# Kernel tuning notes

Hardware: AMD Instinct MI355X
Metric: run time of the kernel (lower is better)

Reference implementation:

```python
import jax, jax.numpy as jnp
import numpy as np

T = 2048
N = 4096
DT = 0.01
V_RESET = 1.0
ALPHA = 0.01
MAX_SPIKES = 128


def setup_inputs() -> dict:
    key = jax.random.key(0)
    ks = jax.random.split(key, 8)
    ts = jnp.arange(T, dtype=jnp.float32) * DT
    input_current = jax.random.normal(ks[0], (T, N), dtype=jnp.float32)
    # _build_w: uniform(minval=0.5) fully-connected weight matrix
    w = jax.random.uniform(ks[1], (N, N), dtype=jnp.float32, minval=0.5, maxval=1.0)
    # _build_initial: uniform(maxval=0.1)
    v0 = jax.random.uniform(ks[2], (N,), dtype=jnp.float32, maxval=0.1)
    i0 = jax.random.uniform(ks[3], (N,), dtype=jnp.float32, maxval=0.1)
    mu = jax.random.uniform(ks[4], (2,), dtype=jnp.float32, minval=0.5, maxval=1.0)
    # uniforms for initial s and for post-spike s resampling (s = log(u) - alpha)
    s0_u = jax.random.uniform(ks[5], (N,), dtype=jnp.float32)
    resample_u = jax.random.uniform(ks[6], (T, N), dtype=jnp.float32)
    return {"ts": ts, "input_current": input_current, "w": w, "v0": v0,
            "i0": i0, "mu": mu, "s0_u": s0_u, "resample_u": resample_u,
            "max_spikes": MAX_SPIKES}


def reference(ts, input_current, w, v0, i0, mu, s0_u, resample_u, max_spikes):
    """Event-driven spiking net: Euler integration of the drift vf with
    spike events when s crosses 0, followed by the masked per-neuron jump
    transition (_inner_trans_fn) using the firing neuron's weight row.
    Returns trajectory ys [T, N, 3] (v, i, s per neuron)."""
    dt = ts[1] - ts[0]
    eps = jnp.float32(1e-12)
    # s0 = log(uniform) - alpha  (always negative; drifts up at rate intensity(v))
    s0 = jnp.log(s0_u + eps) - ALPHA
    y0 = jnp.stack([v0, i0, s0], axis=-1)  # [N, 3]
    mu1, mu2 = mu[0], mu[1]

    def step(carry, xs):
        y, nsp = carry
        inp_t, ru_t = xs
        v, i, s = y[:, 0], y[:, 1], y[:, 2]
        # drift_vf (Euler step)
        v_n = v + dt * (mu1 * (i - v) + mu1 * inp_t)
        i_n = i + dt * (-mu2 * i)
        s_n = s + dt * jax.nn.sigmoid(v)  # intensity_fn(v)
        # event detection: cond_fn = s; event when s reaches 0
        ev = s_n >= 0.0  # [N] event mask
        fire = jnp.any(ev) & (nsp < max_spikes)
        idx = jnp.argmax(ev)  # event_idx = argmax over event mask
        w_row = w[idx]  # weights from firing neuron to all neurons
        # _inner_trans_fn: spiking neurons reset v and resample s;
        # non-spiking neurons receive current injection w[idx][j]
        v_t = jnp.where(ev, v_n - V_RESET, v_n)
        i_t = jnp.where(ev, i_n, i_n + w_row)
        s_t = jnp.where(ev, jnp.log(ru_t + eps) - ALPHA, s_n)
        y_fire = jnp.stack([v_t, i_t, s_t], axis=-1)
        y_free = jnp.stack([v_n, i_n, s_n], axis=-1)
        y_out = jnp.where(fire, y_fire, y_free)
        nsp = nsp + fire.astype(jnp.int32)
        return (y_out, nsp), y_out

    (_, _), ys = jax.lax.scan(step, (y0, jnp.int32(0)),
                              (input_current, resample_u))
    return ys
```

## Files before the change

kernel.cpp:

```cpp
#include <hip/hip_runtime.h>
#include <stddef.h>

#define TT 2048
#define NN 4096
#define LSEG 64
#define NSEG (TT / LSEG)
#define NBLK 16
#define TPB 256
#define MAXU 0xFFFFFFFFu
#define NOFIRE 0xFFFFFFFEu

__global__ __launch_bounds__(TPB) void phaseA(
    const float* __restrict__ ts, const float* __restrict__ inp,
    const float* __restrict__ w, const float* __restrict__ v0,
    const float* __restrict__ i0, const float* __restrict__ mu,
    const float* __restrict__ s0u, const float* __restrict__ ru,
    const int* __restrict__ mx, float* __restrict__ ys,
    unsigned int* __restrict__ hdr, unsigned int* __restrict__ slots)
{
#pragma clang fp contract(off)
  const int tid = threadIdx.x;
  const int n = blockIdx.x * TPB + tid;
  const float dt = ts[1] - ts[0];
  const float mu1 = mu[0], mu2 = mu[1];
  const int maxs = mx[0];

  float v = v0[n];
  float i_nw = i0[n];
  float s = logf(s0u[n] + 1e-12f) - 0.01f;
  float wv = 0.0f;
  bool applyw = false;
  float inpv = inp[n];
  float ruv  = ru[n];
  int nsp = 0;
  int t_stop = TT;

  __shared__ unsigned int sh_w[TPB / 64];
  __shared__ unsigned int sh_b;

  for (int t = 0; t < TT; ++t) {
    float inpv_n = 0.0f, ruv_n = 0.0f;
    if (t + 1 < TT) {
      inpv_n = inp[(size_t)(t + 1) * NN + n];
      ruv_n  = ru[(size_t)(t + 1) * NN + n];
    }
    float logru = logf(ruv + 1e-12f) - 0.01f;
    float sig = 1.0f / (1.0f + expf(-v));
    float sn = s + dt * sig;
    bool ev = sn >= 0.0f;
    bool coupled = (nsp < maxs);

    if (coupled) {
      unsigned int m = ev ? (unsigned int)n : NOFIRE;
#pragma unroll
      for (int off = 32; off > 0; off >>= 1) {
        unsigned int o = (unsigned int)__shfl_down((int)m, off, 64);
        m = m < o ? m : o;
      }
      if ((tid & 63) == 0) sh_w[tid >> 6] = m;
      __syncthreads();
      if (tid == 0) {
        unsigned int bm = sh_w[0];
        for (int k = 1; k < TPB / 64; ++k) bm = bm < sh_w[k] ? bm : sh_w[k];
        __hip_atomic_store(&slots[(size_t)t * NBLK + blockIdx.x], bm,
                           __ATOMIC_RELAXED, __HIP_MEMORY_SCOPE_AGENT);
      }
    }

    float i_full = applyw ? (i_nw + wv) : i_nw;
    if (t > 0) {
      size_t o = ((size_t)(t - 1) * NN + n) * 3;
      ys[o] = v; ys[o + 1] = i_full; ys[o + 2] = s;
    }
    float vn  = v + dt * (mu1 * (i_full - v) + mu1 * inpv);
    float in_ = i_full + dt * (-mu2 * i_full);

    unsigned int gm = NOFIRE;
    if (coupled) {
      if (tid == 0) {
        unsigned int res = NOFIRE;
        long guard = 0;
        for (;;) {
          unsigned int mn = MAXU;
          bool all = true;
#pragma unroll
          for (int bk = 0; bk < NBLK; ++bk) {
            unsigned int x = __hip_atomic_load(&slots[(size_t)t * NBLK + bk],
                                               __ATOMIC_RELAXED,
                                               __HIP_MEMORY_SCOPE_AGENT);
            all = all && (x != MAXU);
            mn = mn < x ? mn : x;
          }
          if (all || ++guard > (1L << 21)) { res = mn; break; }
        }
        sh_b = res;
      }
      __syncthreads();
      gm = sh_b;
    }

    bool fire = coupled && (gm < (unsigned int)NN);
    applyw = false;
    if (fire) {
      nsp += 1;
      wv = w[(size_t)gm * NN + n];
      if (ev) { v = vn - 1.0f; s = logru; }
      else    { v = vn; s = sn; applyw = true; }
    } else {
      v = vn; s = sn;
    }
    i_nw = in_;
    inpv = inpv_n; ruv = ruv_n;

    if (nsp >= maxs && ((t + 1) & (LSEG - 1)) == 0) { t_stop = t + 1; break; }
  }

  {
    float i_full = applyw ? (i_nw + wv) : i_nw;
    size_t o = ((size_t)(t_stop - 1) * NN + n) * 3;
    ys[o] = v; ys[o + 1] = i_full; ys[o + 2] = s;
  }
  if (n == 0) hdr[0] = (unsigned int)t_stop;
}

__global__ __launch_bounds__(TPB) void p1_segc(
    const float* __restrict__ ts, const float* __restrict__ inp,
    const float* __restrict__ mu, const float* __restrict__ ys,
    const unsigned int* __restrict__ hdr, float* __restrict__ buf1)
{
  unsigned int Kp = hdr[0];
  unsigned int g0 = Kp / LSEG;
  unsigned int g = blockIdx.x >> 4;
  if (g < g0) return;
  int n = (blockIdx.x & 15) * TPB + threadIdx.x;
  float dt = ts[1] - ts[0];
  float mu1 = mu[0], mu2 = mu[1];
  float a = 1.0f - dt * mu1, b = dt * mu1, r = 1.0f - dt * mu2;
  float ibase = ys[((size_t)(Kp - 1) * NN + n) * 3 + 1];
  float ij = ibase * powf(r, (float)((int)(g * LSEG) - (int)Kp));
  float c = 0.0f;
  size_t base = (size_t)(g * LSEG) * NN + n;
  for (int j = 0; j < LSEG; ++j) {
    float x = inp[base + (size_t)j * NN];
    c = a * c + b * (ij + x);
    ij *= r;
  }
  buf1[(size_t)g * NN + n] = c;
}

__global__ __launch_bounds__(TPB) void p2_scanv(
    const float* __restrict__ ts, const float* __restrict__ mu,
    const float* __restrict__ ys, const unsigned int* __restrict__ hdr,
    float* __restrict__ buf1)
{
  unsigned int Kp = hdr[0];
  unsigned int g0 = Kp / LSEG;
  if (g0 >= NSEG) return;
  int n = blockIdx.x * TPB + threadIdx.x;
  float dt = ts[1] - ts[0];
  float mu1 = mu[0];
  float a = 1.0f - dt * mu1;
  float aL = a;
  for (int k = 0; k < 6; ++k) aL *= aL;
  float v = ys[((size_t)(Kp - 1) * NN + n) * 3 + 0];
  for (unsigned int g = g0; g < NSEG; ++g) {
    float cg = buf1[(size_t)g * NN + n];
    buf1[(size_t)g * NN + n] = v;
    v = aL * v + cg;
  }
}

__global__ __launch_bounds__(TPB) void p3_seg(
    const float* __restrict__ ts, const float* __restrict__ inp,
    const float* __restrict__ mu, const unsigned int* __restrict__ hdr,
    const float* __restrict__ buf1, float* __restrict__ buf2,
    float* __restrict__ ys)
{
  unsigned int Kp = hdr[0];
  unsigned int g0 = Kp / LSEG;
  unsigned int g = blockIdx.x >> 4;
  if (g < g0) return;
  int n = (blockIdx.x & 15) * TPB + threadIdx.x;
  float dt = ts[1] - ts[0];
  float mu1 = mu[0], mu2 = mu[1];
  float r = 1.0f - dt * mu2;
  float v = buf1[(size_t)g * NN + n];
  float ibase = ys[((size_t)(Kp - 1) * NN + n) * 3 + 1];
  float i = ibase * powf(r, (float)((int)(g * LSEG) - (int)Kp));
  float sl = 0.0f;
  for (int j = 0; j < LSEG; ++j) {
    size_t t = (size_t)g * LSEG + j;
    float x = inp[t * NN + n];
    float sig = 1.0f / (1.0f + expf(-v));
    sl = sl + dt * sig;
    float vn  = v + dt * (mu1 * (i - v) + mu1 * x);
    float in_ = i + dt * (-mu2 * i);
    size_t o = (t * NN + n) * 3;
    ys[o] = vn; ys[o + 1] = in_; ys[o + 2] = sl;
    v = vn; i = in_;
  }
  buf2[(size_t)g * NN + n] = sl;
}

__global__ __launch_bounds__(TPB) void p4_scans(
    const float* __restrict__ ys, const unsigned int* __restrict__ hdr,
    float* __restrict__ buf2)
{
  unsigned int Kp = hdr[0];
  unsigned int g0 = Kp / LSEG;
  if (g0 >= NSEG) return;
  int n = blockIdx.x * TPB + threadIdx.x;
  float s = ys[((size_t)(Kp - 1) * NN + n) * 3 + 2];
  for (unsigned int g = g0; g < NSEG; ++g) {
    float t = buf2[(size_t)g * NN + n];
    buf2[(size_t)g * NN + n] = s;
    s += t;
  }
}

__global__ __launch_bounds__(TPB) void p5_fixs(
    const unsigned int* __restrict__ hdr, const float* __restrict__ buf2,
    float* __restrict__ ys)
{
  unsigned int Kp = hdr[0];
  size_t e = (size_t)Kp * NN + (size_t)blockIdx.x * TPB + threadIdx.x;
  if (e >= (size_t)TT * NN) return;
  unsigned int t = (unsigned int)(e >> 12);
  unsigned int n = (unsigned int)(e & (NN - 1));
  unsigned int g = t >> 6;
  ys[e * 3 + 2] += buf2[(size_t)g * NN + n];
}

extern "C" void kernel_launch(void* const* d_in, const int* in_sizes, int n_in,
                              void* d_out, int out_size, void* d_ws, size_t ws_size,
                              hipStream_t stream)
{
  (void)in_sizes; (void)n_in; (void)out_size; (void)ws_size;
  const float* ts  = (const float*)d_in[0];
  const float* inp = (const float*)d_in[1];
  const float* w   = (const float*)d_in[2];
  const float* v0  = (const float*)d_in[3];
  const float* i0  = (const float*)d_in[4];
  const float* mu  = (const float*)d_in[5];
  const float* s0u = (const float*)d_in[6];
  const float* ru  = (const float*)d_in[7];
  const int*   mx  = (const int*)d_in[8];
  float* ys = (float*)d_out;

  char* wsb = (char*)d_ws;
  unsigned int* hdr   = (unsigned int*)wsb;
  unsigned int* slots = (unsigned int*)(wsb + 1024);
  float* buf1 = (float*)(wsb + 1024 + (size_t)TT * NBLK * 4);
  float* buf2 = buf1 + (size_t)NSEG * NN;

  hipMemsetAsync(slots, 0xFF, (size_t)TT * NBLK * 4, stream);

  phaseA<<<NBLK, TPB, 0, stream>>>(ts, inp, w, v0, i0, mu, s0u, ru, mx, ys, hdr, slots);
  p1_segc<<<NSEG * 16, TPB, 0, stream>>>(ts, inp, mu, ys, hdr, buf1);
  p2_scanv<<<NN / TPB, TPB, 0, stream>>>(ts, mu, ys, hdr, buf1);
  p3_seg<<<NSEG * 16, TPB, 0, stream>>>(ts, inp, mu, hdr, buf1, buf2, ys);
  p4_scans<<<NN / TPB, TPB, 0, stream>>>(ys, hdr, buf2);
  p5_fixs<<<(TT - 128) * NN / TPB, TPB, 0, stream>>>(hdr, buf2, ys);
}
```

Before: 567.5 us.

## Run coupled phase in a single 1024-thread block, dropping cross-block spin sync

The serial spike-coupled phase now runs in one workgroup of 1024 threads, each handling four neurons with float4 loads and stores, instead of 16 blocks that exchanged per-step minimum indices through global atomics and spin-waiting. The global argmin becomes a block-level reduction through double-buffered shared memory with a single barrier per step, and the slot memset is removed. The goal is to remove the global-memory polling latency on every timestep. In exchange all of this phase now runs on a single compute unit with fewer waves hiding memory latency, and each thread does four times the transcendental work.

```diff
diff --git a/kernel.cpp b/kernel.cpp
--- a/kernel.cpp
+++ b/kernel.cpp
@@ -5,122 +5,151 @@
 #define NN 4096
 #define LSEG 64
 #define NSEG (TT / LSEG)
-#define NBLK 16
 #define TPB 256
-#define MAXU 0xFFFFFFFFu
+#define TPA 1024
+#define NPT 4
 #define NOFIRE 0xFFFFFFFEu
 
-__global__ __launch_bounds__(TPB) void phaseA(
+__global__ __launch_bounds__(TPA) void phaseA(
     const float* __restrict__ ts, const float* __restrict__ inp,
     const float* __restrict__ w, const float* __restrict__ v0,
     const float* __restrict__ i0, const float* __restrict__ mu,
     const float* __restrict__ s0u, const float* __restrict__ ru,
     const int* __restrict__ mx, float* __restrict__ ys,
-    unsigned int* __restrict__ hdr, unsigned int* __restrict__ slots)
+    unsigned int* __restrict__ hdr)
 {
 #pragma clang fp contract(off)
   const int tid = threadIdx.x;
-  const int n = blockIdx.x * TPB + tid;
+  const int wid = tid >> 6;
+  const int lane = tid & 63;
   const float dt = ts[1] - ts[0];
   const float mu1 = mu[0], mu2 = mu[1];
   const int maxs = mx[0];
 
-  float v = v0[n];
-  float i_nw = i0[n];
-  float s = logf(s0u[n] + 1e-12f) - 0.01f;
-  float wv = 0.0f;
-  bool applyw = false;
-  float inpv = inp[n];
-  float ruv  = ru[n];
+  const float4* inp4 = (const float4*)inp;
+  const float4* ru4  = (const float4*)ru;
+  const float4* w4   = (const float4*)w;
+
+  float4 v4 = ((const float4*)v0)[tid];
+  float4 i4 = ((const float4*)i0)[tid];
+  float4 s04 = ((const float4*)s0u)[tid];
+
+  float v[NPT]    = {v4.x, v4.y, v4.z, v4.w};
+  float i_nw[NPT] = {i4.x, i4.y, i4.z, i4.w};
+  float s[NPT];
+  {
+    float su[NPT] = {s04.x, s04.y, s04.z, s04.w};
+#pragma unroll
+    for (int k = 0; k < NPT; ++k) s[k] = logf(su[k] + 1e-12f) - 0.01f;
+  }
+  float wv[NPT] = {0.0f, 0.0f, 0.0f, 0.0f};
+  bool  aw[NPT] = {false, false, false, false};
+  float4 inpv = inp4[tid];
+  float4 ruv  = ru4[tid];
   int nsp = 0;
   int t_stop = TT;
 
-  __shared__ unsigned int sh_w[TPB / 64];
-  __shared__ unsigned int sh_b;
+  __shared__ unsigned int shw[2][TPA / 64];
 
   for (int t = 0; t < TT; ++t) {
-    float inpv_n = 0.0f, ruv_n = 0.0f;
+    float4 inpv_n = make_float4(0.f, 0.f, 0.f, 0.f);
+    float4 ruv_n  = make_float4(0.f, 0.f, 0.f, 0.f);
     if (t + 1 < TT) {
-      inpv_n = inp[(size_t)(t + 1) * NN + n];
-      ruv_n  = ru[(size_t)(t + 1) * NN + n];
-    }
-    float logru = logf(ruv + 1e-12f) - 0.01f;
-    float sig = 1.0f / (1.0f + expf(-v));
-    float sn = s + dt * sig;
-    bool ev = sn >= 0.0f;
+      inpv_n = inp4[(size_t)(t + 1) * (NN / 4) + tid];
+      ruv_n  = ru4[(size_t)(t + 1) * (NN / 4) + tid];
+    }
+    float iv[NPT] = {inpv.x, inpv.y, inpv.z, inpv.w};
+    float rv[NPT] = {ruv.x, ruv.y, ruv.z, ruv.w};
+
+    float sn[NPT]; bool ev[NPT];
+#pragma unroll
+    for (int k = 0; k < NPT; ++k) {
+      float sig = 1.0f / (1.0f + expf(-v[k]));
+      sn[k] = s[k] + dt * sig;
+      ev[k] = sn[k] >= 0.0f;
+    }
     bool coupled = (nsp < maxs);
 
+    unsigned int gm = NOFIRE;
     if (coupled) {
-      unsigned int m = ev ? (unsigned int)n : NOFIRE;
+      unsigned int m = NOFIRE;
+#pragma unroll
+      for (int k = 0; k < NPT; ++k) {
+        unsigned int c = ev[k] ? (unsigned int)(tid * NPT + k) : NOFIRE;
+        m = m < c ? m : c;
+      }
 #pragma unroll
       for (int off = 32; off > 0; off >>= 1) {
         unsigned int o = (unsigned int)__shfl_down((int)m, off, 64);
         m = m < o ? m : o;
       }
-      if ((tid & 63) == 0) sh_w[tid >> 6] = m;
+      if (lane == 0) shw[t & 1][wid] = m;
       __syncthreads();
-      if (tid == 0) {
-        unsigned int bm = sh_w[0];
-        for (int k = 1; k < TPB / 64; ++k) bm = bm < sh_w[k] ? bm : sh_w[k];
-        __hip_atomic_store(&slots[(size_t)t * NBLK + blockIdx.x], bm,
-                           __ATOMIC_RELAXED, __HIP_MEMORY_SCOPE_AGENT);
-      }
-    }
-
-    float i_full = applyw ? (i_nw + wv) : i_nw;
+      unsigned int bm = shw[t & 1][0];
+#pragma unroll
+      for (int b = 1; b < TPA / 64; ++b) {
+        unsigned int x = shw[t & 1][b];
+        bm = bm < x ? bm : x;
+      }
+      gm = bm;
+    }
+
+    float ifull[NPT];
+#pragma unroll
+    for (int k = 0; k < NPT; ++k) ifull[k] = aw[k] ? (i_nw[k] + wv[k]) : i_nw[k];
     if (t > 0) {
-      size_t o = ((size_t)(t - 1) * NN + n) * 3;
-      ys[o] = v; ys[o + 1] = i_full; ys[o + 2] = s;
-    }
-    float vn  = v + dt * (mu1 * (i_full - v) + mu1 * inpv);
-    float in_ = i_full + dt * (-mu2 * i_full);
-
-    unsigned int gm = NOFIRE;
-    if (coupled) {
-      if (tid == 0) {
-        unsigned int res = NOFIRE;
-        long guard = 0;
-        for (;;) {
-          unsigned int mn = MAXU;
-          bool all = true;
-#pragma unroll
-          for (int bk = 0; bk < NBLK; ++bk) {
-            unsigned int x = __hip_atomic_load(&slots[(size_t)t * NBLK + bk],
-                                               __ATOMIC_RELAXED,
-                                               __HIP_MEMORY_SCOPE_AGENT);
-            all = all && (x != MAXU);
-            mn = mn < x ? mn : x;
-          }
-          if (all || ++guard > (1L << 21)) { res = mn; break; }
-        }
-        sh_b = res;
-      }
-      __syncthreads();
-      gm = sh_b;
+      size_t o = ((size_t)(t - 1) * NN + (size_t)tid * NPT) * 3;
+      float4* yo = (float4*)(ys + o);
+      yo[0] = make_float4(v[0], ifull[0], s[0], v[1]);
+      yo[1] = make_float4(ifull[1], s[1], v[2], ifull[2]);
+      yo[2] = make_float4(s[2], v[3], ifull[3], s[3]);
+    }
+
+    float vn[NPT], in_[NPT];
+#pragma unroll
+    for (int k = 0; k < NPT; ++k) {
+      vn[k]  = v[k] + dt * (mu1 * (ifull[k] - v[k]) + mu1 * iv[k]);
+      in_[k] = ifull[k] + dt * (-mu2 * ifull[k]);
     }
 
     bool fire = coupled && (gm < (unsigned int)NN);
-    applyw = false;
+#pragma unroll
+    for (int k = 0; k < NPT; ++k) aw[k] = false;
     if (fire) {
       nsp += 1;
-      wv = w[(size_t)gm * NN + n];
-      if (ev) { v = vn - 1.0f; s = logru; }
-      else    { v = vn; s = sn; applyw = true; }
+      float4 wr = w4[(size_t)gm * (NN / 4) + tid];
+      wv[0] = wr.x; wv[1] = wr.y; wv[2] = wr.z; wv[3] = wr.w;
+#pragma unroll
+      for (int k = 0; k < NPT; ++k) {
+        if (ev[k]) {
+          v[k] = vn[k] - 1.0f;
+          s[k] = logf(rv[k] + 1e-12f) - 0.01f;
+        } else {
+          v[k] = vn[k]; s[k] = sn[k]; aw[k] = true;
+        }
+      }
     } else {
-      v = vn; s = sn;
-    }
-    i_nw = in_;
+#pragma unroll
+      for (int k = 0; k < NPT; ++k) { v[k] = vn[k]; s[k] = sn[k]; }
+    }
+#pragma unroll
+    for (int k = 0; k < NPT; ++k) i_nw[k] = in_[k];
     inpv = inpv_n; ruv = ruv_n;
 
     if (nsp >= maxs && ((t + 1) & (LSEG - 1)) == 0) { t_stop = t + 1; break; }
   }
 
   {
-    float i_full = applyw ? (i_nw + wv) : i_nw;
-    size_t o = ((size_t)(t_stop - 1) * NN + n) * 3;
-    ys[o] = v; ys[o + 1] = i_full; ys[o + 2] = s;
-  }
-  if (n == 0) hdr[0] = (unsigned int)t_stop;
+    float ifull[NPT];
+#pragma unroll
+    for (int k = 0; k < NPT; ++k) ifull[k] = aw[k] ? (i_nw[k] + wv[k]) : i_nw[k];
+    size_t o = ((size_t)(t_stop - 1) * NN + (size_t)tid * NPT) * 3;
+    float4* yo = (float4*)(ys + o);
+    yo[0] = make_float4(v[0], ifull[0], s[0], v[1]);
+    yo[1] = make_float4(ifull[1], s[1], v[2], ifull[2]);
+    yo[2] = make_float4(s[2], v[3], ifull[3], s[3]);
+  }
+  if (tid == 0) hdr[0] = (unsigned int)t_stop;
 }
 
 __global__ __launch_bounds__(TPB) void p1_segc(
@@ -248,14 +277,11 @@
   float* ys = (float*)d_out;
 
   char* wsb = (char*)d_ws;
-  unsigned int* hdr   = (unsigned int*)wsb;
-  unsigned int* slots = (unsigned int*)(wsb + 1024);
-  float* buf1 = (float*)(wsb + 1024 + (size_t)TT * NBLK * 4);
+  unsigned int* hdr = (unsigned int*)wsb;
+  float* buf1 = (float*)(wsb + 1024);
   float* buf2 = buf1 + (size_t)NSEG * NN;
 
-  hipMemsetAsync(slots, 0xFF, (size_t)TT * NBLK * 4, stream);
-
-  phaseA<<<NBLK, TPB, 0, stream>>>(ts, inp, w, v0, i0, mu, s0u, ru, mx, ys, hdr, slots);
+  phaseA<<<1, TPA, 0, stream>>>(ts, inp, w, v0, i0, mu, s0u, ru, mx, ys, hdr);
   p1_segc<<<NSEG * 16, TPB, 0, stream>>>(ts, inp, mu, ys, hdr, buf1);
   p2_scanv<<<NN / TPB, TPB, 0, stream>>>(ts, mu, ys, hdr, buf1);
   p3_seg<<<NSEG * 16, TPB, 0, stream>>>(ts, inp, mu, hdr, buf1, buf2, ys);
```

After: 816.9 us. 43.9% more time.
